# Performance work log

Hardware: AMD Instinct MI355X
Metric: run time of the kernel (lower is better)

The kernel has to match this reference:

```python
import jax, jax.numpy as jnp
import numpy as np

B, L, C, H, Wd = 256, 64, 256, 32, 32  # batch, num_filts, code_dim, height, width

def setup_inputs() -> dict:
    key = jax.random.key(0)
    k1, k2 = jax.random.split(key)
    code = jax.random.normal(k1, (B, L, C), dtype=jnp.float32)
    # stacked per-filter weights: weights[l].weight has shape [code_dim, H*W]
    W = jax.random.normal(k2, (L, C, H * Wd), dtype=jnp.float32) * (1.0 / np.sqrt(C))
    return {"code": code, "W": W}

def reference(code, W):
    # Original: for each filter l, x_hat[:, l] = code[:, l, :] @ weights[l].weight
    # (F.linear(x, weight.t()) == x @ weight). Fuse into one batched GEMM.
    # code: [B, L, C], W: [L, C, HW] -> out: [B, L, HW]
    x_hat = jnp.einsum('blc,lcd->bld', code, W)
    return x_hat.reshape(code.shape[0], W.shape[0], H, Wd)
```

## Files before the change

kernel.cpp:

```cpp
#include <hip/hip_runtime.h>
#include <hip/hip_bf16.h>

#define B_  256
#define L_  64
#define C_  256
#define HW_ 1024

typedef float  floatx4 __attribute__((ext_vector_type(4)));
typedef __bf16 bf16x8  __attribute__((ext_vector_type(8)));
typedef __bf16 bf16x4  __attribute__((ext_vector_type(4)));
typedef __bf16 bf16x2  __attribute__((ext_vector_type(2)));

#define LDT_A 72
#define LDB_ROW 128

#define BARRIER_LDS() asm volatile("s_waitcnt lgkmcnt(0)\n\ts_barrier" ::: "memory")

__device__ __forceinline__ int bswz(int n) { return (n ^ (n >> 2)) & 7; }


__device__ __forceinline__ void compute_tile(const __bf16* __restrict__ Albuf,
                                             const unsigned char* __restrict__ Blbuf,
                                             floatx4 (&acc)[4][2],
                                             int lane, int wm, int wn)
{
    #pragma unroll
    for (int ks = 0; ks < 2; ++ks) {
        bf16x8 af[4], bfr[2];
        const int koff = ks * 32 + (lane >> 4) * 8;
        #pragma unroll
        for (int i = 0; i < 4; ++i)
            af[i] = *(const bf16x8*)&Albuf[(wm + i * 16 + (lane & 15)) * LDT_A + koff];
        #pragma unroll
        for (int j = 0; j < 2; ++j) {
            const int n = wn + j * 16 + (lane & 15);
            bfr[j] = *(const bf16x8*)&Blbuf[n * LDB_ROW + (((koff >> 3) ^ bswz(n)) << 4)];
        }
        #pragma unroll
        for (int i = 0; i < 4; ++i)
            #pragma unroll
            for (int j = 0; j < 2; ++j)
                acc[i][j] = __builtin_amdgcn_mfma_f32_16x16x32_bf16(af[i], bfr[j], acc[i][j], 0, 0, 0);
    }
}

__global__ __launch_bounds__(1024, 4)
void gld_mfma_kernel(const float* __restrict__ code,
                     const float* __restrict__ W,
                     float* __restrict__ out)
{
    const int tid = threadIdx.x;

    const int id   = blockIdx.x;
    const int ll   = id & 7;
    const int rest = id >> 3;
    const int n0   = (rest & 7) * 128;
    const int l    = (rest >> 3) * 8 + ll;

    __shared__ __bf16 Alds[2][256 * LDT_A];
    __shared__ unsigned char Blds[2][128 * LDB_ROW];

    const int lane = tid & 63;
    const int wave = tid >> 6;
    const int wm = (wave >> 2) * 64;
    const int wn = (wave & 3) * 32;

    floatx4 acc[4][2];
    #pragma unroll
    for (int i = 0; i < 4; ++i)
        #pragma unroll
        for (int j = 0; j < 2; ++j)
            acc[i][j] = (floatx4)0.0f;

    const int a_row = tid >> 4;
    const int a_kc  = (tid & 15) * 4;
    const int b_i = tid & 31;
    const int b_k = tid >> 5;

    const float* aBase = code + (size_t)l * C_ + a_kc;
    const float* wBase = W + (size_t)l * (C_ * HW_) + (size_t)(2 * b_k) * HW_ + n0 + 4 * b_i;

    floatx4 Areg[2][4];
    floatx4 Breg[2][2];

    #pragma unroll
    for (int p = 0; p < 4; ++p)
        Areg[0][p] = *(const floatx4*)(aBase + (size_t)(p * 64 + a_row) * (L_ * C_));
    #pragma unroll
    for (int r = 0; r < 2; ++r)
        Breg[0][r] = *(const floatx4*)(wBase + (size_t)r * HW_);

    int bwaddr[4];
    #pragma unroll
    for (int j = 0; j < 4; ++j) {
        const int row = 4 * b_i + j;
        bwaddr[j] = row * LDB_ROW + (((b_k >> 2) ^ bswz(row)) << 4) + ((b_k & 3) << 2);
    }

    #pragma unroll
    for (int t = 0; t < 4; ++t) {
        const int s  = t & 1;
        const int kb = t * 64;

        if (t < 3) {
            #pragma unroll
            for (int p = 0; p < 4; ++p)
                Areg[s ^ 1][p] = *(const floatx4*)(aBase + (size_t)(p * 64 + a_row) * (L_ * C_) + (kb + 64));
            #pragma unroll
            for (int r = 0; r < 2; ++r)
                Breg[s ^ 1][r] = *(const floatx4*)(wBase + (size_t)(kb + 64 + r) * HW_);
        }

        if (t > 0)
            compute_tile(Alds[s ^ 1], Blds[s ^ 1], acc, lane, wm, wn);

        #pragma unroll
        for (int j = 0; j < 4; ++j) {
            bf16x2 h;
            h.x = (__bf16)Breg[s][0][j];
            h.y = (__bf16)Breg[s][1][j];
            *(bf16x2*)&Blds[s][bwaddr[j]] = h;
        }
        #pragma unroll
        for (int p = 0; p < 4; ++p) {
            bf16x4 h;
            h.x = (__bf16)Areg[s][p].x; h.y = (__bf16)Areg[s][p].y;
            h.z = (__bf16)Areg[s][p].z; h.w = (__bf16)Areg[s][p].w;
            *(bf16x4*)&Alds[s][(p * 64 + a_row) * LDT_A + a_kc] = h;
        }

        BARRIER_LDS();
    }

    compute_tile(Alds[1], Blds[1], acc, lane, wm, wn);

    const int col0 = lane & 15;
    const int row0 = (lane >> 4) * 4;
    #pragma unroll
    for (int i = 0; i < 4; ++i) {
        #pragma unroll
        for (int j = 0; j < 2; ++j) {
            const int m = wm + i * 16 + row0;
            const int n = n0 + wn + j * 16 + col0;
            float* o = out + (size_t)m * (L_ * HW_) + (size_t)l * HW_ + n;
            #pragma unroll
            for (int r = 0; r < 4; ++r)
                o[(size_t)r * (L_ * HW_)] = acc[i][j][r];
        }
    }
}

extern "C" void kernel_launch(void* const* d_in, const int* in_sizes, int n_in,
                              void* d_out, int out_size, void* d_ws, size_t ws_size,
                              hipStream_t stream) {
    const float* code = (const float*)d_in[0];
    const float* W    = (const float*)d_in[1];
    float* out        = (float*)d_out;

    gld_mfma_kernel<<<dim3(512), 1024, 0, stream>>>(code, W, out);
}
```

Before: 130.0 us.

## Widen N tile to 256 and halve K step to 32 per stage

Each block now computes a 256x256 output tile (up from 256x128), so each wave holds a 4x4 MFMA accumulator set, and the grid drops to 256 blocks. The K loop runs 8 stages of 32 instead of 4 stages of 64, which shrinks the LDS buffers and uses a new row padding and swizzle. The goal is to reload the code (A) operand half as often and raise MFMA work per LDS load. In exchange, only 256 blocks exist for the whole device, more stages mean more barriers, and the larger accumulator set raises register pressure under the 1024-thread launch bound.

```diff
diff --git a/kernel.cpp b/kernel.cpp
--- a/kernel.cpp
+++ b/kernel.cpp
@@ -11,38 +11,12 @@
 typedef __bf16 bf16x4  __attribute__((ext_vector_type(4)));
 typedef __bf16 bf16x2  __attribute__((ext_vector_type(2)));
 
-#define LDT_A 72
-#define LDB_ROW 128
+#define LDA_ROW 80
+#define LDB_ROW 64
 
 #define BARRIER_LDS() asm volatile("s_waitcnt lgkmcnt(0)\n\ts_barrier" ::: "memory")
 
-__device__ __forceinline__ int bswz(int n) { return (n ^ (n >> 2)) & 7; }
-
-
-__device__ __forceinline__ void compute_tile(const __bf16* __restrict__ Albuf,
-                                             const unsigned char* __restrict__ Blbuf,
-                                             floatx4 (&acc)[4][2],
-                                             int lane, int wm, int wn)
-{
-    #pragma unroll
-    for (int ks = 0; ks < 2; ++ks) {
-        bf16x8 af[4], bfr[2];
-        const int koff = ks * 32 + (lane >> 4) * 8;
-        #pragma unroll
-        for (int i = 0; i < 4; ++i)
-            af[i] = *(const bf16x8*)&Albuf[(wm + i * 16 + (lane & 15)) * LDT_A + koff];
-        #pragma unroll
-        for (int j = 0; j < 2; ++j) {
-            const int n = wn + j * 16 + (lane & 15);
-            bfr[j] = *(const bf16x8*)&Blbuf[n * LDB_ROW + (((koff >> 3) ^ bswz(n)) << 4)];
-        }
-        #pragma unroll
-        for (int i = 0; i < 4; ++i)
-            #pragma unroll
-            for (int j = 0; j < 2; ++j)
-                acc[i][j] = __builtin_amdgcn_mfma_f32_16x16x32_bf16(af[i], bfr[j], acc[i][j], 0, 0, 0);
-    }
-}
+__device__ __forceinline__ int g2(int n) { return (n ^ (n >> 2)) & 3; }
 
 __global__ __launch_bounds__(1024, 4)
 void gld_mfma_kernel(const float* __restrict__ code,
@@ -54,38 +28,36 @@
     const int id   = blockIdx.x;
     const int ll   = id & 7;
     const int rest = id >> 3;
-    const int n0   = (rest & 7) * 128;
-    const int l    = (rest >> 3) * 8 + ll;
+    const int n0   = (rest & 3) * 256;
+    const int l    = (rest >> 2) * 8 + ll;
 
-    __shared__ __bf16 Alds[2][256 * LDT_A];
-    __shared__ unsigned char Blds[2][128 * LDB_ROW];
+    __shared__ unsigned char Alds[2][256 * LDA_ROW];
+    __shared__ unsigned char Blds[2][256 * LDB_ROW];
 
     const int lane = tid & 63;
     const int wave = tid >> 6;
     const int wm = (wave >> 2) * 64;
-    const int wn = (wave & 3) * 32;
+    const int wn = (wave & 3) * 64;
 
-    floatx4 acc[4][2];
+    floatx4 acc[4][4];
     #pragma unroll
     for (int i = 0; i < 4; ++i)
         #pragma unroll
-        for (int j = 0; j < 2; ++j)
+        for (int j = 0; j < 4; ++j)
             acc[i][j] = (floatx4)0.0f;
 
-    const int a_row = tid >> 4;
-    const int a_kc  = (tid & 15) * 4;
-    const int b_i = tid & 31;
-    const int b_k = tid >> 5;
+    const int a_row = tid >> 2;
+    const int a_k4  = (tid & 3) * 4;
+    const int b_i = tid & 63;
 
-    const float* aBase = code + (size_t)l * C_ + a_kc;
-    const float* wBase = W + (size_t)l * (C_ * HW_) + (size_t)(2 * b_k) * HW_ + n0 + 4 * b_i;
+    const float* aBase = code + (size_t)l * C_ + a_k4;
+    const float* wBase = W + (size_t)l * (C_ * HW_) + (size_t)(2 * wave) * HW_ + n0 + 4 * b_i;
 
-    floatx4 Areg[2][4];
+    floatx4 Areg[2][2];
     floatx4 Breg[2][2];
 
-    #pragma unroll
-    for (int p = 0; p < 4; ++p)
-        Areg[0][p] = *(const floatx4*)(aBase + (size_t)(p * 64 + a_row) * (L_ * C_));
+    Areg[0][0] = *(const floatx4*)(aBase + (size_t)a_row * (L_ * C_));
+    Areg[0][1] = *(const floatx4*)(aBase + (size_t)a_row * (L_ * C_) + 16);
     #pragma unroll
     for (int r = 0; r < 2; ++r)
         Breg[0][r] = *(const floatx4*)(wBase + (size_t)r * HW_);
@@ -94,25 +66,42 @@
     #pragma unroll
     for (int j = 0; j < 4; ++j) {
         const int row = 4 * b_i + j;
-        bwaddr[j] = row * LDB_ROW + (((b_k >> 2) ^ bswz(row)) << 4) + ((b_k & 3) << 2);
+        bwaddr[j] = row * LDB_ROW + ((((wave >> 2) ^ g2(row))) << 4) + ((wave & 3) << 2);
     }
+    const int awaddr = a_row * LDA_ROW + 2 * a_k4;
 
     #pragma unroll
-    for (int t = 0; t < 4; ++t) {
+    for (int t = 0; t < 8; ++t) {
         const int s  = t & 1;
-        const int kb = t * 64;
+        const int kb = t * 32;
 
-        if (t < 3) {
-            #pragma unroll
-            for (int p = 0; p < 4; ++p)
-                Areg[s ^ 1][p] = *(const floatx4*)(aBase + (size_t)(p * 64 + a_row) * (L_ * C_) + (kb + 64));
+        if (t < 7) {
+            Areg[s ^ 1][0] = *(const floatx4*)(aBase + (size_t)a_row * (L_ * C_) + (kb + 32));
+            Areg[s ^ 1][1] = *(const floatx4*)(aBase + (size_t)a_row * (L_ * C_) + (kb + 48));
             #pragma unroll
             for (int r = 0; r < 2; ++r)
-                Breg[s ^ 1][r] = *(const floatx4*)(wBase + (size_t)(kb + 64 + r) * HW_);
+                Breg[s ^ 1][r] = *(const floatx4*)(wBase + (size_t)(kb + 32 + r) * HW_);
         }
 
-        if (t > 0)
-            compute_tile(Alds[s ^ 1], Blds[s ^ 1], acc, lane, wm, wn);
+        if (t > 0) {
+            const unsigned char* Ab = Alds[s ^ 1];
+            const unsigned char* Bb = Blds[s ^ 1];
+            bf16x8 af[4], bfr[4];
+            const int c16 = lane >> 4;
+            #pragma unroll
+            for (int i = 0; i < 4; ++i)
+                af[i] = *(const bf16x8*)&Ab[(wm + i * 16 + (lane & 15)) * LDA_ROW + c16 * 16];
+            #pragma unroll
+            for (int j = 0; j < 4; ++j) {
+                const int n = wn + j * 16 + (lane & 15);
+                bfr[j] = *(const bf16x8*)&Bb[n * LDB_ROW + ((c16 ^ g2(n)) << 4)];
+            }
+            #pragma unroll
+            for (int i = 0; i < 4; ++i)
+                #pragma unroll
+                for (int j = 0; j < 4; ++j)
+                    acc[i][j] = __builtin_amdgcn_mfma_f32_16x16x32_bf16(af[i], bfr[j], acc[i][j], 0, 0, 0);
+        }
 
         #pragma unroll
         for (int j = 0; j < 4; ++j) {
@@ -122,24 +111,42 @@
             *(bf16x2*)&Blds[s][bwaddr[j]] = h;
         }
         #pragma unroll
-        for (int p = 0; p < 4; ++p) {
+        for (int p = 0; p < 2; ++p) {
             bf16x4 h;
             h.x = (__bf16)Areg[s][p].x; h.y = (__bf16)Areg[s][p].y;
             h.z = (__bf16)Areg[s][p].z; h.w = (__bf16)Areg[s][p].w;
-            *(bf16x4*)&Alds[s][(p * 64 + a_row) * LDT_A + a_kc] = h;
+            *(bf16x4*)&Alds[s][awaddr + p * 32] = h;
         }
 
         BARRIER_LDS();
     }
 
-    compute_tile(Alds[1], Blds[1], acc, lane, wm, wn);
+    {
+        const unsigned char* Ab = Alds[1];
+        const unsigned char* Bb = Blds[1];
+        bf16x8 af[4], bfr[4];
+        const int c16 = lane >> 4;
+        #pragma unroll
+        for (int i = 0; i < 4; ++i)
+            af[i] = *(const bf16x8*)&Ab[(wm + i * 16 + (lane & 15)) * LDA_ROW + c16 * 16];
+        #pragma unroll
+        for (int j = 0; j < 4; ++j) {
+            const int n = wn + j * 16 + (lane & 15);
+            bfr[j] = *(const bf16x8*)&Bb[n * LDB_ROW + ((c16 ^ g2(n)) << 4)];
+        }
+        #pragma unroll
+        for (int i = 0; i < 4; ++i)
+            #pragma unroll
+            for (int j = 0; j < 4; ++j)
+                acc[i][j] = __builtin_amdgcn_mfma_f32_16x16x32_bf16(af[i], bfr[j], acc[i][j], 0, 0, 0);
+    }
 
     const int col0 = lane & 15;
     const int row0 = (lane >> 4) * 4;
     #pragma unroll
     for (int i = 0; i < 4; ++i) {
         #pragma unroll
-        for (int j = 0; j < 2; ++j) {
+        for (int j = 0; j < 4; ++j) {
             const int m = wm + i * 16 + row0;
             const int n = n0 + wn + j * 16 + col0;
             float* o = out + (size_t)m * (L_ * HW_) + (size_t)l * HW_ + n;
@@ -157,5 +164,5 @@
     const float* W    = (const float*)d_in[1];
     float* out        = (float*)d_out;
 
-    gld_mfma_kernel<<<dim3(512), 1024, 0, stream>>>(code, W, out);
+    gld_mfma_kernel<<<dim3(256), 1024, 0, stream>>>(code, W, out);
 }
```

Result: faster. 124.7 us (-4.0%).
